# Kernel optimization log

Hardware: AMD Instinct MI355X
Metric: run time of the kernel (lower is better)

Reference implementation:

```python
import jax, jax.numpy as jnp
import numpy as np

N = 100000
E = 1600000
D_IN = 128
D_HID = 128

def setup_inputs() -> dict:
    key = jax.random.key(0)
    ks = jax.random.split(key, 8)
    x = jax.random.normal(ks[0], (N, D_IN), dtype=jnp.float32)
    edge_index = jax.random.randint(ks[1], (2, E), 0, N, dtype=jnp.int32)
    edge_weight = jax.random.uniform(ks[2], (E,), dtype=jnp.float32)
    W1 = jax.random.normal(ks[3], (D_IN, D_HID), dtype=jnp.float32) / np.sqrt(D_IN)
    b1 = jnp.zeros((D_HID,), dtype=jnp.float32)
    W2 = jax.random.normal(ks[4], (D_HID, D_HID), dtype=jnp.float32) / np.sqrt(D_HID)
    b2 = jnp.zeros((D_HID,), dtype=jnp.float32)
    W3 = jax.random.normal(ks[5], (D_HID, 1), dtype=jnp.float32) / np.sqrt(D_HID)
    b3 = jnp.zeros((1,), dtype=jnp.float32)
    return {"x": x, "edge_index": edge_index, "edge_weight": edge_weight,
            "W1": W1, "b1": b1, "W2": W2, "b2": b2, "W3": W3, "b3": b3}

def _gcn_norm(edge_index, edge_weight, n):
    # Add self-loops (weight 1) and compute symmetric normalization, as in PyG GCNConv.
    loop = jnp.arange(n, dtype=edge_index.dtype)
    src = jnp.concatenate([edge_index[0], loop])
    dst = jnp.concatenate([edge_index[1], loop])
    w = jnp.concatenate([edge_weight, jnp.ones((n,), edge_weight.dtype)])
    deg = jax.ops.segment_sum(w, dst, num_segments=n)  # [N]
    dis = jnp.where(deg > 0, jax.lax.rsqrt(jnp.where(deg > 0, deg, 1.0)), 0.0)
    norm = dis[src] * w * dis[dst]  # [E+N]
    return src, dst, norm

def _gcn_conv(x, W, b, src, dst, norm, n):
    h = x @ W  # [N, out]
    msg = norm[:, None] * h[src]  # gather + scale, [E+N, out]
    out = jax.ops.segment_sum(msg, dst, num_segments=n)  # scatter-add
    return out + b

def reference(x, edge_index, edge_weight, W1, b1, W2, b2, W3, b3):
    n = x.shape[0]
    src, dst, norm = _gcn_norm(edge_index, edge_weight, n)
    h = jax.nn.relu(_gcn_conv(x, W1, b1, src, dst, norm, n))
    h = jax.nn.relu(_gcn_conv(h, W2, b2, src, dst, norm, n))
    h = _gcn_conv(h, W3, b3, src, dst, norm, n)
    return jax.nn.relu(h).squeeze(-1)  # [N]
```

## Files before the change

### kernel.cpp

```cpp
#include <hip/hip_runtime.h>
#include <hip/hip_fp16.h>
#include <math.h>

#define NFEAT 128
#define CAP 64
#define BINSHIFT 7
#define GB 256

typedef int2 EdgeRec;

__device__ inline float4 h4_to_f4(uint2 u) {
  __half2 lo = *(__half2*)&u.x;
  __half2 hi = *(__half2*)&u.y;
  float2 a = __half22float2(lo), b = __half22float2(hi);
  return make_float4(a.x, a.y, b.x, b.y);
}
__device__ inline uint2 f4_to_h4(float4 v) {
  __half2 lo = __floats2half2_rn(v.x, v.y);
  __half2 hi = __floats2half2_rn(v.z, v.w);
  uint2 r; r.x = *(unsigned*)&lo; r.y = *(unsigned*)&hi; return r;
}


__global__ __launch_bounds__(256) void k_hist(const int* __restrict__ dst,
                                              unsigned* __restrict__ histG,
                                              int E, int EPB, int nbins) {
  __shared__ unsigned lh[1024];
  for (int i = threadIdx.x; i < nbins; i += 256) lh[i] = 0;
  __syncthreads();
  int start = blockIdx.x * EPB;
  int end = start + EPB; if (end > E) end = E;
  for (int e = start + threadIdx.x; e < end; e += 256)
    atomicAdd(&lh[dst[e] >> BINSHIFT], 1u);
  __syncthreads();
  for (int i = threadIdx.x; i < nbins; i += 256)
    histG[(size_t)blockIdx.x * nbins + i] = lh[i];
}

__global__ __launch_bounds__(1024) void k_scan(unsigned* __restrict__ histG,
                                               unsigned* __restrict__ binBase,
                                               int nbins) {
  __shared__ unsigned tot[1024];
  int b = threadIdx.x;
  unsigned running = 0;
  if (b < nbins)
    for (int blk = 0; blk < GB; blk++) running += histG[(size_t)blk * nbins + b];
  tot[b] = (b < nbins) ? running : 0;
  __syncthreads();
  for (int off = 1; off < 1024; off <<= 1) {
    unsigned v = (b >= off) ? tot[b - off] : 0;
    __syncthreads();
    tot[b] += v;
    __syncthreads();
  }
  unsigned base = (b == 0) ? 0u : tot[b - 1];
  if (b < nbins) binBase[b] = base;
  if (b == 0) binBase[nbins] = tot[1023];
  if (b < nbins) {
    unsigned run = base;
    for (int blk = 0; blk < GB; blk++) {
      unsigned v = histG[(size_t)blk * nbins + b];
      histG[(size_t)blk * nbins + b] = run;
      run += v;
    }
  }
}

__global__ __launch_bounds__(256) void k_scatter(const int* __restrict__ src,
                                                 const int* __restrict__ dst,
                                                 const float* __restrict__ ew,
                                                 const unsigned* __restrict__ histG,
                                                 uint2* __restrict__ sorted,
                                                 int E, int EPB, int nbins) {
  __shared__ unsigned lrank[1024];
  __shared__ unsigned lbase[1024];
  for (int i = threadIdx.x; i < nbins; i += 256) {
    lrank[i] = 0;
    lbase[i] = histG[(size_t)blockIdx.x * nbins + i];
  }
  __syncthreads();
  int start = blockIdx.x * EPB;
  int end = start + EPB; if (end > E) end = E;
  for (int e = start + threadIdx.x; e < end; e += 256) {
    int d = dst[e];
    int bin = d >> BINSHIFT;
    unsigned r = atomicAdd(&lrank[bin], 1u);
    uint2 rec;
    rec.x = (unsigned)src[e] | ((unsigned)(d & 127) << 24);
    rec.y = __float_as_uint(ew[e]);
    sorted[lbase[bin] + r] = rec;
  }
}

__global__ __launch_bounds__(256) void k_csr(const uint2* __restrict__ sorted,
                                             const unsigned* __restrict__ binBase,
                                             unsigned* __restrict__ cnt,
                                             EdgeRec* __restrict__ ep,
                                             float* __restrict__ dis, int N) {
  int bin = blockIdx.x;
  __shared__ unsigned lcnt[128];
  __shared__ float lsum[128];
  if (threadIdx.x < 128) { lcnt[threadIdx.x] = 0; lsum[threadIdx.x] = 0.f; }
  __syncthreads();
  unsigned s0 = binBase[bin], s1 = binBase[bin + 1];
  int node0 = bin << BINSHIFT;
  for (unsigned e = s0 + threadIdx.x; e < s1; e += 256) {
    uint2 rec = sorted[e];
    int dlow = rec.x >> 24;
    int srcn = rec.x & 0xFFFFFF;
    unsigned slot = atomicAdd(&lcnt[dlow], 1u);
    EdgeRec r; r.x = srcn; r.y = (int)rec.y;
    ep[(size_t)(node0 + dlow) * CAP + slot] = r;
    atomicAdd(&lsum[dlow], __uint_as_float(rec.y));
  }
  __syncthreads();
  if (threadIdx.x < 128) {
    int node = node0 + threadIdx.x;
    if (node < N) {
      cnt[node] = lcnt[threadIdx.x];
      dis[node] = 1.0f / sqrtf(1.0f + lsum[threadIdx.x]);
    }
  }
}

__global__ __launch_bounds__(256) void k_premul(EdgeRec* __restrict__ ep,
                                                const unsigned* __restrict__ cnt,
                                                const float* __restrict__ dis, int N) {
  int wave = threadIdx.x >> 6;
  int lane = threadIdx.x & 63;
  int node = blockIdx.x * 4 + wave;
  if (node >= N) return;
  int c = (int)cnt[node];
  if (lane < c) {
    int e = node * CAP + lane;
    EdgeRec r = ep[e];
    r.y = __float_as_int(dis[r.x] * __int_as_float(r.y));
    ep[e] = r;
  }
}


__global__ __launch_bounds__(1024) void k_gemm1(const float* __restrict__ X,
                                                const float* __restrict__ W,
                                                __half* __restrict__ Y,
                                                int N, int numTiles) {
  __shared__ float sW[128 * 128];
  __shared__ float sX[128 * 128];
  int t = threadIdx.x;
  int wave = __builtin_amdgcn_readfirstlane(t >> 6);
  int lane = t & 63;
  int lr = (lane >> 3) & 7;
  int lc = lane & 7;
  int wr = wave >> 2;
  int wc = wave & 3;

  {
    const float4* W4 = (const float4*)W;
    float4* sW4 = (float4*)sW;
    for (int i = t; i < 4096; i += 1024) sW4[i] = W4[i];
  }

  const float4* X4 = (const float4*)X;
  int grmax = N - 1;
  int r0 = wr * 32 + lr * 4;
  int c0 = wc * 32 + lc * 4;
  int swzk = ((r0 >> 2) & 7) << 2;

  for (int tile = blockIdx.x; tile < numTiles; tile += gridDim.x) {
    int rowBase = tile * 128;
    __syncthreads();
    {
      int kg = t & 31;
      int rb = t >> 5;
#pragma unroll
      for (int p = 0; p < 4; p++) {
        int r = rb + 32 * p;
        int gr = rowBase + r; if (gr > grmax) gr = grmax;
        float4 v = X4[(size_t)gr * 32 + kg];
        int swz = ((r >> 2) & 7) << 2;
        *(float4*)(&sX[r * 128 + ((kg * 4) ^ swz)]) = v;
      }
    }
    __syncthreads();

    float4 acc[4];
#pragma unroll
    for (int i = 0; i < 4; i++) acc[i] = make_float4(0.f, 0.f, 0.f, 0.f);

#pragma unroll 1
    for (int kg = 0; kg < 32; kg++) {
      int kk0 = kg * 4;
      float4 xf[4];
#pragma unroll
      for (int i = 0; i < 4; i++)
        xf[i] = *(const float4*)(&sX[(r0 + i) * 128 + (kk0 ^ swzk)]);
      float4 wf[4];
#pragma unroll
      for (int kk = 0; kk < 4; kk++)
        wf[kk] = *(const float4*)(&sW[(kk0 + kk) * 128 + c0]);
#pragma unroll
      for (int kk = 0; kk < 4; kk++) {
#pragma unroll
        for (int i = 0; i < 4; i++) {
          float xs = (&xf[i].x)[kk];
          acc[i].x = fmaf(xs, wf[kk].x, acc[i].x);
          acc[i].y = fmaf(xs, wf[kk].y, acc[i].y);
          acc[i].z = fmaf(xs, wf[kk].z, acc[i].z);
          acc[i].w = fmaf(xs, wf[kk].w, acc[i].w);
        }
      }
    }

#pragma unroll
    for (int i = 0; i < 4; i++) {
      int row = rowBase + r0 + i;
      if (row < N)
        *(uint2*)(Y + (size_t)row * 128 + c0) = f4_to_h4(acc[i]);
    }
  }
}


__global__ __launch_bounds__(1024) void k_aggemm(const __half* __restrict__ H,
                                                 const unsigned* __restrict__ cntA,
                                                 const EdgeRec* __restrict__ ep,
                                                 const float* __restrict__ dis,
                                                 const float* __restrict__ bias,
                                                 const float* __restrict__ Wm,
                                                 __half* __restrict__ Y,
                                                 int N, int numTiles) {
  __shared__ float sW[128 * 128];
  __shared__ float sX[2][64 * 128];
  int t = threadIdx.x;
  int wave = __builtin_amdgcn_readfirstlane(t >> 6);
  int lane = t & 63;

  {
    const float4* W4 = (const float4*)Wm;
    float4* sW4 = (float4*)sW;
    for (int i = t; i < 4096; i += 1024) sW4[i] = W4[i];
  }
  __syncthreads();

  int gw = wave;
  int half = lane >> 5;
  int l32 = lane & 31;
  int mw = wave - 12;
  int wr = (mw >> 1) & 1;
  int wc = mw & 1;
  int lr = (lane >> 3) & 7;
  int lc = lane & 7;
  int rB = wr * 32 + lr * 4;
  int cA = wc * 64 + lc * 4;
  int cB = cA + 32;
  int swzm = lr << 2;
  int s2b = 2 * gw;

  for (int it = 0;; it++) {
    int gtile = blockIdx.x + it * gridDim.x;
    int mtile = gtile - (int)gridDim.x;
    bool anyG = gtile < numTiles;
    bool anyM = (it >= 1) && (mtile < numTiles);
    if (!anyG && !anyM) break;

    if (wave < 12) {
      if (anyG) {
        float* buf = sX[it & 1];
        int tileBase = gtile * 64;
        int cnts[3];
#pragma unroll
        for (int k = 0; k < 3; k++) {
          int s2 = s2b + 24 * k;
          int node = tileBase + s2 + half;
          int nodec = node < N ? node : N - 1;
          unsigned pk = cntA[nodec];
          cnts[k] = (s2 < 64 && node < N) ? (int)pk : 0;
        }
#pragma unroll 1
        for (int k = 0; k < 3; k++) {
          int s2 = s2b + 24 * k;
          if (s2 >= 64) break;
          int node = tileBase + s2 + half;
          int cnt = cnts[k];
          int beg = (node < N ? node : 0) * CAP;
          int last = beg + cnt - 1;

          float4 acc = make_float4(0.f, 0.f, 0.f, 0.f);
          if (cnt > 0) {
            EdgeRec e0[4], e1[4], e2[4], e3[4];
            uint2 h0[4], h1[4];
#pragma unroll
            for (int q = 0; q < 4; q++) { int e = beg + q;     e0[q] = ep[e <= last ? e : last]; }
#pragma unroll
            for (int q = 0; q < 4; q++) { int e = beg + 4 + q; e1[q] = ep[e <= last ? e : last]; }
#pragma unroll
            for (int q = 0; q < 4; q++) { int e = beg + 8 + q; e2[q] = ep[e <= last ? e : last]; }
#pragma unroll
            for (int q = 0; q < 4; q++)
              h0[q] = *(const uint2*)(H + (size_t)e0[q].x * 128 + 4 * l32);
#pragma unroll
            for (int q = 0; q < 4; q++)
              h1[q] = *(const uint2*)(H + (size_t)e1[q].x * 128 + 4 * l32);
            for (int p = 0; p < cnt; p += 4) {
              uint2 h2[4];
#pragma unroll
              for (int q = 0; q < 4; q++) {
                int e = beg + p + 12 + q;
                e3[q] = ep[e <= last ? e : last];
              }
#pragma unroll
              for (int q = 0; q < 4; q++)
                h2[q] = *(const uint2*)(H + (size_t)e2[q].x * 128 + 4 * l32);
#pragma unroll
              for (int q = 0; q < 4; q++) {
                float w = (p + q < cnt) ? __int_as_float(e0[q].y) : 0.f;
                float4 hv = h4_to_f4(h0[q]);
                acc.x = fmaf(w, hv.x, acc.x);
                acc.y = fmaf(w, hv.y, acc.y);
                acc.z = fmaf(w, hv.z, acc.z);
                acc.w = fmaf(w, hv.w, acc.w);
              }
#pragma unroll
              for (int q = 0; q < 4; q++) {
                e0[q] = e1[q]; e1[q] = e2[q]; e2[q] = e3[q];
                h0[q] = h1[q]; h1[q] = h2[q];
              }
            }
          }
          if (node < N) {
            float ds = dis[node];
            float4 hn = h4_to_f4(*(const uint2*)(H + (size_t)node * 128 + 4 * l32));
            acc.x = fmaf(ds, hn.x, acc.x);
            acc.y = fmaf(ds, hn.y, acc.y);
            acc.z = fmaf(ds, hn.z, acc.z);
            acc.w = fmaf(ds, hn.w, acc.w);
            float4 bv = *(const float4*)(bias + 4 * l32);
            float4 o;
            o.x = fmaf(ds, acc.x, bv.x); o.x = o.x > 0.f ? o.x : 0.f;
            o.y = fmaf(ds, acc.y, bv.y); o.y = o.y > 0.f ? o.y : 0.f;
            o.z = fmaf(ds, acc.z, bv.z); o.z = o.z > 0.f ? o.z : 0.f;
            o.w = fmaf(ds, acc.w, bv.w); o.w = o.w > 0.f ? o.w : 0.f;
            int s = s2 + half;
            int swz = ((s >> 2) & 7) << 2;
            *(float4*)(&buf[s * 128 + ((4 * l32) ^ swz)]) = o;
          }
        }
      }
    } else {
      if (anyM) {
        const float* buf = sX[(it - 1) & 1];
        float4 accA[4], accB[4];
#pragma unroll
        for (int i = 0; i < 4; i++) {
          accA[i] = make_float4(0.f, 0.f, 0.f, 0.f);
          accB[i] = make_float4(0.f, 0.f, 0.f, 0.f);
        }
#pragma unroll 2
        for (int kg = 0; kg < 32; kg++) {
          int kk0 = kg * 4;
          float4 xf[4];
#pragma unroll
          for (int i = 0; i < 4; i++)
            xf[i] = *(const float4*)(&buf[(rB + i) * 128 + (kk0 ^ swzm)]);
#pragma unroll
          for (int kk = 0; kk < 4; kk++) {
            float4 wA = *(const float4*)(&sW[(kk0 + kk) * 128 + cA]);
            float4 wB = *(const float4*)(&sW[(kk0 + kk) * 128 + cB]);
#pragma unroll
            for (int i = 0; i < 4; i++) {
              float xs = (&xf[i].x)[kk];
              accA[i].x = fmaf(xs, wA.x, accA[i].x);
              accA[i].y = fmaf(xs, wA.y, accA[i].y);
              accA[i].z = fmaf(xs, wA.z, accA[i].z);
              accA[i].w = fmaf(xs, wA.w, accA[i].w);
              accB[i].x = fmaf(xs, wB.x, accB[i].x);
              accB[i].y = fmaf(xs, wB.y, accB[i].y);
              accB[i].z = fmaf(xs, wB.z, accB[i].z);
              accB[i].w = fmaf(xs, wB.w, accB[i].w);
            }
          }
        }
        int rowBase = mtile * 64;
#pragma unroll
        for (int i = 0; i < 4; i++) {
          int row = rowBase + rB + i;
          if (row < N) {
            *(uint2*)(Y + (size_t)row * 128 + cA) = f4_to_h4(accA[i]);
            *(uint2*)(Y + (size_t)row * 128 + cB) = f4_to_h4(accB[i]);
          }
        }
      }
    }
    __syncthreads();
  }
}


__global__ __launch_bounds__(256) void k_agg_final(const __half* __restrict__ H,
                                                   const unsigned* __restrict__ cntA,
                                                   const EdgeRec* __restrict__ ep,
                                                   const float* __restrict__ dis,
                                                   const float* __restrict__ bias,
                                                   const float* __restrict__ W3,
                                                   float* __restrict__ z, int N) {
  int wave = __builtin_amdgcn_readfirstlane(threadIdx.x >> 6);
  int lane = threadIdx.x & 63;
  int half = lane >> 5;
  int l32  = lane & 31;
  int node = blockIdx.x * 8 + wave * 2 + half;
  int nodec = node < N ? node : N - 1;
  int cnt = (node < N) ? (int)cntA[nodec] : 0;
  int beg = nodec * CAP;
  int last = beg + cnt - 1;

  float4 acc = make_float4(0.f, 0.f, 0.f, 0.f);
  if (cnt > 0) {
    EdgeRec e0[4], e1[4], e2[4];
    uint2 h0[4], h1[4];
#pragma unroll
    for (int q = 0; q < 4; q++) { int e = beg + q;     e0[q] = ep[e <= last ? e : last]; }
#pragma unroll
    for (int q = 0; q < 4; q++) { int e = beg + 4 + q; e1[q] = ep[e <= last ? e : last]; }
#pragma unroll
    for (int q = 0; q < 4; q++)
      h0[q] = *(const uint2*)(H + (size_t)e0[q].x * 128 + 4 * l32);
    for (int p = 0; p < cnt; p += 4) {
      uint2 h1n[4];
#pragma unroll
      for (int q = 0; q < 4; q++) {
        int e = beg + p + 8 + q;
        e2[q] = ep[e <= last ? e : last];
      }
#pragma unroll
      for (int q = 0; q < 4; q++)
        h1n[q] = *(const uint2*)(H + (size_t)e1[q].x * 128 + 4 * l32);
#pragma unroll
      for (int q = 0; q < 4; q++) {
        float w = (p + q < cnt) ? __int_as_float(e0[q].y) : 0.f;
        float4 hv = h4_to_f4(h0[q]);
        acc.x = fmaf(w, hv.x, acc.x);
        acc.y = fmaf(w, hv.y, acc.y);
        acc.z = fmaf(w, hv.z, acc.z);
        acc.w = fmaf(w, hv.w, acc.w);
      }
#pragma unroll
      for (int q = 0; q < 4; q++) { e0[q] = e1[q]; e1[q] = e2[q]; h0[q] = h1n[q]; }
    }
  }
  float ds = dis[nodec];
  float4 hn = h4_to_f4(*(const uint2*)(H + (size_t)nodec * 128 + 4 * l32));
  acc.x = fmaf(ds, hn.x, acc.x);
  acc.y = fmaf(ds, hn.y, acc.y);
  acc.z = fmaf(ds, hn.z, acc.z);
  acc.w = fmaf(ds, hn.w, acc.w);
  float4 bv = *(const float4*)(bias + 4 * l32);
  float4 w3v = *(const float4*)(W3 + 4 * l32);
  float o, pdot = 0.f;
  o = fmaf(ds, acc.x, bv.x); o = o > 0.f ? o : 0.f; pdot = fmaf(o, w3v.x, pdot);
  o = fmaf(ds, acc.y, bv.y); o = o > 0.f ? o : 0.f; pdot = fmaf(o, w3v.y, pdot);
  o = fmaf(ds, acc.z, bv.z); o = o > 0.f ? o : 0.f; pdot = fmaf(o, w3v.z, pdot);
  o = fmaf(ds, acc.w, bv.w); o = o > 0.f ? o : 0.f; pdot = fmaf(o, w3v.w, pdot);
#pragma unroll
  for (int off = 16; off > 0; off >>= 1) pdot += __shfl_down(pdot, off, 32);
  if (l32 == 0 && node < N) z[node] = pdot;
}


__global__ void k_aggs(const float* __restrict__ z, const unsigned* __restrict__ cntA,
                       const EdgeRec* __restrict__ ep, const float* __restrict__ dis,
                       const float* __restrict__ b3, float* __restrict__ out, int N) {
  int n = blockIdx.x * blockDim.x + threadIdx.x;
  if (n >= N) return;
  int cnt = (int)cntA[n];
  float dsn = dis[n];
  float acc = dsn * z[n];
  int beg = n * CAP;
#pragma unroll 4
  for (int e = beg; e < beg + cnt; e++) {
    EdgeRec p = ep[e];
    acc = fmaf(__int_as_float(p.y), z[p.x], acc);
  }
  acc = fmaf(dsn, acc, b3[0]);
  out[n] = acc > 0.f ? acc : 0.f;
}


extern "C" void kernel_launch(void* const* d_in, const int* in_sizes, int n_in,
                              void* d_out, int out_size, void* d_ws, size_t ws_size,
                              hipStream_t stream) {
  const float* x  = (const float*)d_in[0];
  const int*   ei = (const int*)d_in[1];
  const float* ew = (const float*)d_in[2];
  const float* W1 = (const float*)d_in[3];
  const float* b1 = (const float*)d_in[4];
  const float* W2 = (const float*)d_in[5];
  const float* b2 = (const float*)d_in[6];
  const float* W3 = (const float*)d_in[7];
  const float* b3 = (const float*)d_in[8];
  int N = in_sizes[0] / NFEAT;
  int E = in_sizes[2];
  const int* srcp = ei;
  const int* dstp = ei + E;

  char* p = (char*)d_ws;
  auto carve = [&](size_t bytes) -> void* {
    void* r = (void*)p;
    p += (bytes + 511) & ~(size_t)511;
    return r;
  };
  int nbins = (N + 127) >> BINSHIFT;
  unsigned* cnt     = (unsigned*)carve(sizeof(unsigned) * N);
  float*    dis     = (float*)carve(sizeof(float) * N);
  EdgeRec*  ep      = (EdgeRec*)carve(sizeof(EdgeRec) * (size_t)N * CAP);
  __half*   t1      = (__half*)carve(sizeof(__half) * (size_t)N * NFEAT);
  __half*   t2      = (__half*)carve(sizeof(__half) * (size_t)N * NFEAT);
  float*    z       = (float*)carve(sizeof(float) * N);
  unsigned* histG   = (unsigned*)carve(sizeof(unsigned) * (size_t)GB * nbins);
  unsigned* binBase = (unsigned*)carve(sizeof(unsigned) * (nbins + 1));
  uint2*    sorted  = (uint2*)carve(sizeof(uint2) * (size_t)E);

  int gN = (N + 255) / 256;
  int numTiles128 = (N + 127) / 128;
  int numTiles64  = (N + 63) / 64;
  int GG = 256;
  int EPB = (E + GB - 1) / GB;
  int gP = (N + 3) / 4;
  int gF = (N + 7) / 8;

  k_hist<<<GB, 256, 0, stream>>>(dstp, histG, E, EPB, nbins);
  k_scan<<<1, 1024, 0, stream>>>(histG, binBase, nbins);
  k_scatter<<<GB, 256, 0, stream>>>(srcp, dstp, ew, histG, sorted, E, EPB, nbins);
  k_csr<<<nbins, 256, 0, stream>>>(sorted, binBase, cnt, ep, dis, N);
  k_gemm1<<<GG, 1024, 0, stream>>>(x, W1, t1, N, numTiles128);
  k_premul<<<gP, 256, 0, stream>>>(ep, cnt, dis, N);
  k_aggemm<<<GG, 1024, 0, stream>>>(t1, cnt, ep, dis, b1, W2, t2, N, numTiles64);
  k_agg_final<<<gF, 256, 0, stream>>>(t2, cnt, ep, dis, b2, W3, z, N);
  k_aggs<<<gN, 256, 0, stream>>>(z, cnt, ep, dis, b3, (float*)d_out, N);
}
```

Baseline: 473.0 us.

## Parallelize bin-offset scan across blocks with transposed histogram layout

The per-block histogram is stored bin-major so each bin's block counts are contiguous. A single-block serial scan that looped over all blocks per bin is replaced by three kernels: per-bin wavefront reductions, a single-block scan of bin totals, and a per-bin wavefront exclusive scan that writes per-block offsets. This removes a long serial, uncoalesced loop run by one workgroup, at the cost of two extra kernel launches. The scatter kernel reads its offsets from the new layout.

```diff
diff --git a/kernel.cpp b/kernel.cpp
--- a/kernel.cpp
+++ b/kernel.cpp
@@ -34,18 +34,27 @@
     atomicAdd(&lh[dst[e] >> BINSHIFT], 1u);
   __syncthreads();
   for (int i = threadIdx.x; i < nbins; i += 256)
-    histG[(size_t)blockIdx.x * nbins + i] = lh[i];
-}
-
-__global__ __launch_bounds__(1024) void k_scan(unsigned* __restrict__ histG,
-                                               unsigned* __restrict__ binBase,
-                                               int nbins) {
+    histG[(size_t)i * GB + blockIdx.x] = lh[i];
+}
+
+__global__ __launch_bounds__(256) void k_scanT(const unsigned* __restrict__ histG,
+                                               unsigned* __restrict__ binTot, int nbins) {
+  int wave = threadIdx.x >> 6;
+  int lane = threadIdx.x & 63;
+  int bin = blockIdx.x * 4 + wave;
+  if (bin >= nbins) return;
+  uint4 v = *(const uint4*)(histG + (size_t)bin * GB + lane * 4);
+  int s = (int)(v.x + v.y + v.z + v.w);
+#pragma unroll
+  for (int off = 32; off > 0; off >>= 1) s += __shfl_down(s, off, 64);
+  if (lane == 0) binTot[bin] = (unsigned)s;
+}
+
+__global__ __launch_bounds__(1024) void k_scanB(const unsigned* __restrict__ binTot,
+                                                unsigned* __restrict__ binBase, int nbins) {
   __shared__ unsigned tot[1024];
   int b = threadIdx.x;
-  unsigned running = 0;
-  if (b < nbins)
-    for (int blk = 0; blk < GB; blk++) running += histG[(size_t)blk * nbins + b];
-  tot[b] = (b < nbins) ? running : 0;
+  tot[b] = (b < nbins) ? binTot[b] : 0;
   __syncthreads();
   for (int off = 1; off < 1024; off <<= 1) {
     unsigned v = (b >= off) ? tot[b - off] : 0;
@@ -53,17 +62,34 @@
     tot[b] += v;
     __syncthreads();
   }
-  unsigned base = (b == 0) ? 0u : tot[b - 1];
-  if (b < nbins) binBase[b] = base;
+  if (b < nbins) binBase[b] = (b == 0) ? 0u : tot[b - 1];
   if (b == 0) binBase[nbins] = tot[1023];
-  if (b < nbins) {
-    unsigned run = base;
-    for (int blk = 0; blk < GB; blk++) {
-      unsigned v = histG[(size_t)blk * nbins + b];
-      histG[(size_t)blk * nbins + b] = run;
-      run += v;
-    }
-  }
+}
+
+__global__ __launch_bounds__(256) void k_scanC(unsigned* __restrict__ histG,
+                                               const unsigned* __restrict__ binBase,
+                                               int nbins) {
+  int wave = threadIdx.x >> 6;
+  int lane = threadIdx.x & 63;
+  int bin = blockIdx.x * 4 + wave;
+  if (bin >= nbins) return;
+  uint4 v = *(const uint4*)(histG + (size_t)bin * GB + lane * 4);
+  unsigned i1 = v.x + v.y;
+  unsigned i2 = i1 + v.z;
+  unsigned i3 = i2 + v.w;
+  int inc = (int)i3;
+#pragma unroll
+  for (int off = 1; off < 64; off <<= 1) {
+    int t = __shfl_up(inc, off, 64);
+    if (lane >= off) inc += t;
+  }
+  unsigned base = binBase[bin] + (unsigned)inc - i3;
+  uint4 o;
+  o.x = base;
+  o.y = base + v.x;
+  o.z = base + i1;
+  o.w = base + i2;
+  *(uint4*)(histG + (size_t)bin * GB + lane * 4) = o;
 }
 
 __global__ __launch_bounds__(256) void k_scatter(const int* __restrict__ src,
@@ -76,7 +102,7 @@
   __shared__ unsigned lbase[1024];
   for (int i = threadIdx.x; i < nbins; i += 256) {
     lrank[i] = 0;
-    lbase[i] = histG[(size_t)blockIdx.x * nbins + i];
+    lbase[i] = histG[(size_t)i * GB + blockIdx.x];
   }
   __syncthreads();
   int start = blockIdx.x * EPB;
@@ -516,6 +542,7 @@
   __half*   t2      = (__half*)carve(sizeof(__half) * (size_t)N * NFEAT);
   float*    z       = (float*)carve(sizeof(float) * N);
   unsigned* histG   = (unsigned*)carve(sizeof(unsigned) * (size_t)GB * nbins);
+  unsigned* binTot  = (unsigned*)carve(sizeof(unsigned) * nbins);
   unsigned* binBase = (unsigned*)carve(sizeof(unsigned) * (nbins + 1));
   uint2*    sorted  = (uint2*)carve(sizeof(uint2) * (size_t)E);
 
@@ -524,11 +551,14 @@
   int numTiles64  = (N + 63) / 64;
   int GG = 256;
   int EPB = (E + GB - 1) / GB;
+  int gS = (nbins + 3) / 4;
   int gP = (N + 3) / 4;
   int gF = (N + 7) / 8;
 
   k_hist<<<GB, 256, 0, stream>>>(dstp, histG, E, EPB, nbins);
-  k_scan<<<1, 1024, 0, stream>>>(histG, binBase, nbins);
+  k_scanT<<<gS, 256, 0, stream>>>(histG, binTot, nbins);
+  k_scanB<<<1, 1024, 0, stream>>>(binTot, binBase, nbins);
+  k_scanC<<<gS, 256, 0, stream>>>(histG, binBase, nbins);
   k_scatter<<<GB, 256, 0, stream>>>(srcp, dstp, ew, histG, sorted, E, EPB, nbins);
   k_csr<<<nbins, 256, 0, stream>>>(sorted, binBase, cnt, ep, dis, N);
   k_gemm1<<<GG, 1024, 0, stream>>>(x, W1, t1, N, numTiles128);
```

Result: faster. 430.7 us (-9.0%).
